# Optimization experiments

Measured on AMD Instinct MI355X. Metric: run time of the kernel, lower is better.

## Reference

```python
import jax, jax.numpy as jnp
import numpy as np

# ---- static config (matches init_kwargs: nlevs=[2,3,4], Pyr_mode=1, dfilt='pkva') ----
NLEVS = (2, 3, 4)
L = 3
# symmetric length-12 ladder (lifting) filter in the spirit of the 'pkva' ladder filter
_PKVA_HALF = np.array([0.6300, -0.1930, 0.0972, -0.0526, 0.0272, -0.0144])
PKVA = np.concatenate([_PKVA_HALF[::-1], _PKVA_HALF])


def _lp_hp_masks(H, W):
    """Meyer-style smooth lowpass/highpass frequency masks (rcos smooth_func)."""
    def phi(n):
        w = np.abs(2.0 * np.pi * np.fft.fftfreq(n))
        s = np.clip((w - np.pi / 3.0) / (np.pi / 3.0), 0.0, 1.0)
        beta = s ** 4 * (35.0 - 84.0 * s + 70.0 * s ** 2 - 20.0 * s ** 3)
        return np.cos(0.5 * np.pi * beta)
    Lm = phi(H)[:, None] * phi(W)[None, :]
    Hm = np.sqrt(np.clip(1.0 - Lm ** 2, 0.0, None))
    return jnp.asarray(Lm, jnp.float32), jnp.asarray(Hm, jnp.float32)


def _pyr_dec(x, nlev):
    """PyrNDDEC_mm, Pyr_mode=1: FFT-domain smooth LP/HP split, dyadic decimation of LP."""
    bands = []
    for _ in range(nlev):
        H, W = x.shape[-2], x.shape[-1]
        Lm, Hm = _lp_hp_masks(H, W)
        Xf = jnp.fft.fft2(x)
        bands.append(jnp.fft.ifft2(Xf * Hm).real.astype(x.dtype))
        x = jnp.fft.ifft2(Xf * Lm).real.astype(x.dtype)[..., ::2, ::2]
    return [x] + bands[::-1]  # y[0]=coarsest lowpass, y[1..L]=bandpass coarse->fine


def _conv1d_wrap(x, f, axis):
    """1D circular ('wrap') convolution along `axis`."""
    K = f.shape[0]
    x = jnp.moveaxis(x, axis, -1)
    pad = [(0, 0)] * (x.ndim - 1) + [(K // 2, K - 1 - K // 2)]
    xp = jnp.pad(x, pad, mode='wrap')
    shp = xp.shape
    y = jax.lax.conv_general_dilated(xp.reshape(-1, 1, shp[-1]),
                                     f.reshape(1, 1, K).astype(x.dtype), (1,), 'VALID')
    y = y.reshape(shp[:-1] + (shp[-1] - K + 1,))
    return jnp.moveaxis(y, -1, axis)


def _fan_split(x, axis, f):
    """One ladder-structured fan filter-bank stage with quincunx coset split."""
    other = -2 if axis == -1 else -1
    n_other = x.shape[other]
    shape = [1] * x.ndim
    shape[other] = n_other
    idx = jnp.arange(n_other)
    # fan <-> diamond modulation along the other axis
    sign = (1 - 2 * (idx % 2)).astype(x.dtype).reshape(shape)
    xm = x * sign
    # quincunx cosets: shift odd lines by 1 along split axis, then deinterleave
    parity = ((idx % 2) == 1).reshape(shape)
    xs = jnp.where(parity, jnp.roll(xm, -1, axis=axis), xm)
    if axis == -1:
        p0, p1 = xs[..., 0::2], xs[..., 1::2]
    else:
        p0, p1 = xs[..., 0::2, :], xs[..., 1::2, :]
    # ladder (lifting) predict/update with 1D filter f
    d = p1 - _conv1d_wrap(p0, f, axis)
    s = p0 + 0.5 * _conv1d_wrap(d, f, axis)
    return s, d


def _dfbdec(x, f, n):
    """n-level directional filter bank (ladder structure). Returns (2^n, ...) stack."""
    subs = x[None]  # (M, B, 1, H, W), all subbands same shape per level -> vectorized
    axis = -1
    for _ in range(n):
        s, d = _fan_split(subs, axis, f)
        subs = jnp.concatenate([s, d], axis=0)
        axis = -2 if axis == -1 else -1
    return subs


def setup_inputs() -> dict:
    key = jax.random.key(0)
    x = jax.random.normal(key, (16, 1, 1024, 1024), dtype=jnp.float32)
    return {"x": x}


def reference(x):
    f = jnp.asarray(PKVA, x.dtype)
    y = _pyr_dec(x, L)
    outs = [y[0]]  # coarsest lowpass (B,1,128,128)
    for k in range(1, L + 1):
        outs.append(_dfbdec(y[k], f, NLEVS[k - 1]))
    # (lowpass, 4 dirs @128x128, 8 dirs @(256,128), 16 dirs @(256,256))
    return tuple(outs)
```

## Files before the change

### kernel.cpp

```cpp
#include <hip/hip_runtime.h>
#include <math.h>

#define PI_F 3.14159265358979323846f

__constant__ float c_pkva[12] = {
  -0.0144f, 0.0272f, -0.0526f, 0.0972f, -0.193f, 0.63f,
   0.63f, -0.193f, 0.0972f, -0.0526f, 0.0272f, -0.0144f
};

constexpr int ilog2c(int n) { int l = 0; while (n > 1) { n >>= 1; ++l; } return l; }

__device__ float g_phi[1920];
constexpr int phi_off(int N) {
  return (N == 1024) ? 0 : (N == 512) ? 1024 : (N == 256) ? 1536 : 1792;
}

__device__ __forceinline__ float phi_dev(int k, int n) {
  int kk = (k < n - k) ? k : (n - k);
  float w = 2.0f * PI_F * (float)kk / (float)n;
  float s = (w - PI_F / 3.0f) * (3.0f / PI_F);
  s = fminf(fmaxf(s, 0.0f), 1.0f);
  float s2 = s * s;
  float beta = s2 * s2 * (35.0f - 84.0f * s + 70.0f * s2 - 20.0f * s2 * s);
  return __cosf(0.5f * PI_F * beta);
}

__global__ void phi_init_k() {
  int i = blockIdx.x * 256 + threadIdx.x;
  if (i < 1024)      g_phi[i] = phi_dev(i, 1024);
  else if (i < 1536) g_phi[i] = phi_dev(i - 1024, 512);
  else if (i < 1792) g_phi[i] = phi_dev(i - 1536, 256);
  else if (i < 1920) g_phi[i] = phi_dev(i - 1792, 128);
}

__device__ __forceinline__ float2 cmul(float2 a, float2 b) {
  return make_float2(a.x * b.x - a.y * b.y, a.x * b.y + a.y * b.x);
}
__device__ __forceinline__ float2 cadd(float2 a, float2 b) { return make_float2(a.x + b.x, a.y + b.y); }
__device__ __forceinline__ float2 csub(float2 a, float2 b) { return make_float2(a.x - b.x, a.y - b.y); }

template <int N>
__device__ __forceinline__ int fft_core4(float2 (*sbuf)[N], float dirsign, int tid, int cur) {
  constexpr int LOG2 = ilog2c(N);
  constexpr int NT = N / 4;
  constexpr bool LEAD2 = (LOG2 & 1);
  if constexpr (LEAD2) {
#pragma unroll
    for (int j = tid; j < N / 2; j += NT) {
      float2 v0 = sbuf[cur][j], v1 = sbuf[cur][j + N / 2];
      float2 e = cadd(v0, v1), o = csub(v0, v1);
      *(float4*)&sbuf[cur ^ 1][2 * j] = make_float4(e.x, e.y, o.x, o.y);
    }
    cur ^= 1;
    __syncthreads();
  }
#pragma unroll
  for (int Ns = LEAD2 ? 2 : 1; Ns < N; Ns <<= 2) {
    int j = tid;
    int base = j & (Ns - 1);
    float ang = dirsign * (2.0f * PI_F) * (float)base / (float)(4 * Ns);
    float2 w1; __sincosf(ang, &w1.y, &w1.x);
    float2 w2 = cmul(w1, w1);
    float2 w3 = cmul(w2, w1);
    float2 v0 = sbuf[cur][j];
    float2 v1 = cmul(sbuf[cur][j + N / 4], w1);
    float2 v2 = cmul(sbuf[cur][j + N / 2], w2);
    float2 v3 = cmul(sbuf[cur][j + 3 * (N / 4)], w3);
    float2 a0 = cadd(v0, v2), a1 = csub(v0, v2);
    float2 a2 = cadd(v1, v3), a3 = csub(v1, v3);
    float2 r1 = make_float2(-dirsign * a3.y, dirsign * a3.x);
    int idxD = ((j - base) << 2) + base;
    cur ^= 1;
    sbuf[cur][idxD]          = cadd(a0, a2);
    sbuf[cur][idxD + Ns]     = cadd(a1, r1);
    sbuf[cur][idxD + 2 * Ns] = csub(a0, a2);
    sbuf[cur][idxD + 3 * Ns] = csub(a1, r1);
    __syncthreads();
  }
  return cur;
}

template <int N, int LMODE, int SMODE>
__global__ void __launch_bounds__(N / 4)
fft_rows_k(const void* __restrict__ vin, void* __restrict__ vout,
           float dirsign, float scale) {
  constexpr int NT = N / 4;
  __shared__ __align__(16) float2 sbuf[2][N];
  const int tid = threadIdx.x;
  const int row = blockIdx.x;
  const int r = row & (N - 1);

  if (LMODE == 1) {
    const float2* in = (const float2*)vin;
#pragma unroll
    for (int i = tid; i < N; i += NT) {
      float2 v = in[(size_t)row * N + i];
      sbuf[0][i] = make_float2(v.x * scale, v.y * scale);
    }
  } else {
    const float2* in = (const float2*)vin;
    float pr = g_phi[phi_off(N) + r];
#pragma unroll
    for (int i = tid; i < N; i += NT) {
      float lm = pr * g_phi[phi_off(N) + i];
      float m = sqrtf(fmaxf(1.0f - lm * lm, 0.0f)) * scale;
      float2 v = in[(size_t)row * N + i];
      sbuf[0][i] = make_float2(v.x * m, v.y * m);
    }
  }
  __syncthreads();

  int cur = fft_core4<N>(sbuf, dirsign, tid, 0);

  if (SMODE == 0) {
    float2* outp = (float2*)vout;
#pragma unroll
    for (int i = tid; i < N; i += NT)
      outp[(size_t)row * N + i] = sbuf[cur][i];
  } else {
    float* outp = (float*)vout;
#pragma unroll
    for (int i = tid; i < N; i += NT)
      outp[(size_t)row * N + i] = sbuf[cur][i].x;
  }
}

template <int N, int PITCH>
__global__ void __launch_bounds__(N / 4)
rfft_pairs_cm_k(const float* __restrict__ in, float2* __restrict__ out) {
  constexpr int NT = N / 4;
  __shared__ __align__(16) float2 sbuf[2][N];
  const int tid = threadIdx.x;
  const int img = blockIdx.x >> (ilog2c(N) - 1);
  const int b = blockIdx.x & (N / 2 - 1);
  const int r = ((b & 7) << (ilog2c(N) - 4)) + (b >> 3);
  const float* p0 = in + ((size_t)img * N + 2 * r) * N;
  const float* p1 = p0 + N;

#pragma unroll
  for (int i = tid; i < N; i += NT)
    sbuf[0][i] = make_float2(p0[i], p1[i]);
  __syncthreads();

  int cur = fft_core4<N>(sbuf, -1.0f, tid, 0);

  float2* ob = out + (size_t)img * ((size_t)PITCH * N) + 2 * r;
#pragma unroll
  for (int i = tid; i <= N / 2; i += NT) {
    float2 Z = sbuf[cur][i];
    float2 Zr = sbuf[cur][(N - i) & (N - 1)];
    float2 Zc = make_float2(Zr.x, -Zr.y);
    float2 o0 = make_float2(0.5f * (Z.x + Zc.x), 0.5f * (Z.y + Zc.y));
    float2 dd = make_float2(Z.x - Zc.x, Z.y - Zc.y);
    float2 o1 = make_float2(0.5f * dd.y, -0.5f * dd.x);
    *(float4*)&ob[(size_t)i * N] = make_float4(o0.x, o0.y, o1.x, o1.y);
  }
}

__global__ void transpose_rect_k(const float2* __restrict__ in,
                                 float2* __restrict__ out, int R, int C) {
  __shared__ float2 tile[32][33];
  int img = blockIdx.z;
  size_t base = (size_t)img * R * C;
  int c = blockIdx.x * 32 + threadIdx.x;
  int r0 = blockIdx.y * 32;
  for (int j = threadIdx.y; j < 32; j += 8)
    tile[j][threadIdx.x] = in[base + (size_t)(r0 + j) * C + c];
  __syncthreads();
  int r = blockIdx.y * 32 + threadIdx.x;
  int c0 = blockIdx.x * 32;
  for (int j = threadIdx.y; j < 32; j += 8)
    out[base + (size_t)(c0 + j) * R + r] = tile[threadIdx.x][j];
}

template <int N, int PITCH>
__global__ void __launch_bounds__(N / 4)
fft_col_half_k(float2* __restrict__ inout, float2* __restrict__ foldb) {
  constexpr int NT = N / 4;
  constexpr int NH = N / 2;
  __shared__ __align__(16) float2 sbuf[2][N];
  const int tid = threadIdx.x;
  const int kx = blockIdx.x;
  const int img = blockIdx.y;
  float2* rowp = inout + ((size_t)img * PITCH + kx) * N;

#pragma unroll
  for (int i = tid; i < N; i += NT)
    sbuf[0][i] = rowp[i];
  __syncthreads();

  int cur = fft_core4<N>(sbuf, -1.0f, tid, 0);

  const float pr = g_phi[phi_off(N) + kx];
  const float inv = 1.0f / (float)N;
  float2* fp = foldb + ((size_t)img * (NH + 1) + kx) * NH;
#pragma unroll
  for (int i = tid; i < NH; i += NT) {
    float2 vA = sbuf[cur][i];
    float2 vB = sbuf[cur][i + NH];
    float lmA = pr * g_phi[phi_off(N) + i];
    float lmB = pr * g_phi[phi_off(N) + i + NH];
    fp[i] = make_float2(0.25f * (vA.x * lmA + vB.x * lmB),
                        0.25f * (vA.y * lmA + vB.y * lmB));
    float hmA = sqrtf(fmaxf(1.0f - lmA * lmA, 0.0f)) * inv;
    float hmB = sqrtf(fmaxf(1.0f - lmB * lmB, 0.0f)) * inv;
    sbuf[cur][i]      = make_float2(vA.x * hmA, vA.y * hmA);
    sbuf[cur][i + NH] = make_float2(vB.x * hmB, vB.y * hmB);
  }
  __syncthreads();

  cur = fft_core4<N>(sbuf, 1.0f, tid, cur);

#pragma unroll
  for (int i = tid; i < N; i += NT)
    rowp[i] = sbuf[cur][i];
}

__global__ void __launch_bounds__(256)
fold_alias_k(const float2* __restrict__ fold, float2* __restrict__ spec2,
             float2* __restrict__ spec3) {
  __shared__ float2 s2a[512], s2b[512];
  const int rp = blockIdx.x;
  const int img = blockIdx.y;
  const float2* fb = fold + (size_t)img * (513 * 512);
  const float2* fr0 = fb + (size_t)rp * 512;
  const float2* fr1 = fb + (size_t)(512 - rp) * 512;
  const float2* fr2 = fb + (size_t)(rp + 256) * 512;
  const float2* fr3 = fb + (size_t)(256 - rp) * 512;
  float2* sp2 = spec2 + ((size_t)img << 18);
  for (int c = threadIdx.x; c < 512; c += 256) {
    int mc = (512 - c) & 511;
    float2 a0 = fr0[c], b0 = fr1[mc];
    float2 a1 = fr2[c], b1 = fr3[mc];
    float2 v0 = make_float2(a0.x + b0.x, a0.y - b0.y);
    float2 v1 = make_float2(a1.x + b1.x, a1.y - b1.y);
    s2a[c] = v0; s2b[c] = v1;
    sp2[((size_t)rp << 9) + c] = v0;
    sp2[((size_t)(rp + 256) << 9) + c] = v1;
  }
  __syncthreads();
  float pr0 = g_phi[phi_off(512) + rp], pr1 = g_phi[phi_off(512) + rp + 256];
  float2* sp3 = spec3 + ((size_t)img << 16) + ((size_t)rp << 8);
  {
    int c = threadIdx.x;
    float pc0 = g_phi[phi_off(512) + c], pc1 = g_phi[phi_off(512) + c + 256];
    float2 v00 = s2a[c], v01 = s2a[c + 256], v10 = s2b[c], v11 = s2b[c + 256];
    float m00 = pr0 * pc0, m01 = pr0 * pc1, m10 = pr1 * pc0, m11 = pr1 * pc1;
    sp3[c] = make_float2(
        0.25f * (v00.x * m00 + v01.x * m01 + v10.x * m10 + v11.x * m11),
        0.25f * (v00.y * m00 + v01.y * m01 + v10.y * m10 + v11.y * m11));
  }
}

template <int N, int PITCH>
__global__ void __launch_bounds__(N / 4)
ifft_fan_pair_k(const float2* __restrict__ in, float* __restrict__ outb,
                float scale, int halfT) {
  constexpr int NT = N / 4;
  constexpr int W2 = N / 2;
  __shared__ __align__(16) float2 sbuf[2][N];
  const int tid = threadIdx.x;
  const int img = blockIdx.x >> (ilog2c(N) - 1);
  const int q = blockIdx.x & (N / 2 - 1);
  const int y0 = 2 * q;
  const float2* inA = in + ((size_t)img * N + y0) * PITCH;
  const float2* inB = inA + PITCH;

#pragma unroll
  for (int i = tid; i <= W2; i += NT) {
    float2 a = inA[i], b = inB[i];
    sbuf[0][i] = make_float2((a.x - b.y) * scale, (a.y + b.x) * scale);
  }
#pragma unroll
  for (int i = tid; i < W2 - 1; i += NT) {
    int m = W2 - 1 - i;
    float2 a = inA[m], b = inB[m];
    sbuf[0][W2 + 1 + i] = make_float2((a.x + b.y) * scale, (b.x - a.y) * scale);
  }
  __syncthreads();

  int cur = fft_core4<N>(sbuf, 1.0f, tid, 0);

  float* scratch = (float*)sbuf[cur ^ 1];
  float* xe = scratch;
  float* xo = scratch + W2;
  float* db = scratch + 2 * W2;
  const size_t rbase = ((size_t)img * N + y0) * W2;

  for (int sub = 0; sub < 2; ++sub) {
    const int par = sub;
    const float sgn = par ? -1.0f : 1.0f;
#pragma unroll
    for (int i = tid; i < N; i += NT) {
      float v = par ? sbuf[cur][i].y : sbuf[cur][i].x;
      int ii = (i - par) & (N - 1);
      if (ii & 1) xo[ii >> 1] = v; else xe[ii >> 1] = v;
    }
    __syncthreads();

    float* outs = outb + rbase + (size_t)sub * W2;
    float* outd = outb + halfT + rbase + (size_t)sub * W2;
#pragma unroll 2
    for (int j = tid; j < W2; j += NT) {
      float acc = 0.0f;
#pragma unroll
      for (int k = 0; k < 12; k++)
        acc += c_pkva[k] * xe[(j - 6 + k + W2) & (W2 - 1)];
      float dv = sgn * (xo[j] - acc);
      db[j] = dv;
      outd[j] = dv;
    }
    __syncthreads();
#pragma unroll 2
    for (int j = tid; j < W2; j += NT) {
      float acc = 0.0f;
#pragma unroll
      for (int k = 0; k < 12; k++)
        acc += c_pkva[k] * db[(j - 6 + k + W2) & (W2 - 1)];
      outs[j] = sgn * xe[j] + 0.5f * acc;
    }
    __syncthreads();
  }
}

template <int N>
__global__ void __launch_bounds__(N / 4)
ifft_fan_k(const float2* __restrict__ in, float* __restrict__ outb,
           float scale, int halfT) {
  constexpr int NT = N / 4;
  constexpr int W2 = N / 2;
  __shared__ __align__(16) float2 sbuf[2][N];
  const int tid = threadIdx.x;
  const int nr = blockIdx.x;
  const int r = nr & (N - 1);
  const int par = r & 1;
  const float sgn = par ? -1.0f : 1.0f;

#pragma unroll
  for (int i = tid; i < N; i += NT) {
    float2 v = in[(size_t)nr * N + i];
    sbuf[0][i] = make_float2(v.x * scale, v.y * scale);
  }
  __syncthreads();

  int cur = fft_core4<N>(sbuf, 1.0f, tid, 0);

  float* scratch = (float*)sbuf[cur ^ 1];
  float* xe = scratch;
  float* xo = scratch + W2;
  float* db = scratch + 2 * W2;
#pragma unroll
  for (int i = tid; i < N; i += NT) {
    float v = sbuf[cur][i].x;
    int ii = (i - par) & (N - 1);
    if (ii & 1) xo[ii >> 1] = v; else xe[ii >> 1] = v;
  }
  __syncthreads();

  float* outs = outb + (size_t)nr * W2;
  float* outd = outb + halfT + (size_t)nr * W2;
#pragma unroll 2
  for (int j = tid; j < W2; j += NT) {
    float acc = 0.0f;
#pragma unroll
    for (int k = 0; k < 12; k++)
      acc += c_pkva[k] * xe[(j - 6 + k + W2) & (W2 - 1)];
    float dv = sgn * (xo[j] - acc);
    db[j] = dv;
    outd[j] = dv;
  }
  __syncthreads();
#pragma unroll 2
  for (int j = tid; j < W2; j += NT) {
    float acc = 0.0f;
#pragma unroll
    for (int k = 0; k < 12; k++)
      acc += c_pkva[k] * db[(j - 6 + k + W2) & (W2 - 1)];
    outs[j] = sgn * xe[j] + 0.5f * acc;
  }
}

__global__ void transpose_k(const float2* __restrict__ in,
                            float2* __restrict__ out, int N) {
  __shared__ float2 tile[32][33];
  int img = blockIdx.z;
  size_t base = (size_t)img * N * N;
  int x = blockIdx.x * 32 + threadIdx.x;
  int y0 = blockIdx.y * 32;
  for (int j = threadIdx.y; j < 32; j += 8)
    tile[j][threadIdx.x] = in[base + (size_t)(y0 + j) * N + x];
  __syncthreads();
  int x2 = blockIdx.y * 32 + threadIdx.x;
  int y2 = blockIdx.x * 32;
  for (int j = threadIdx.y; j < 32; j += 8)
    out[base + (size_t)(y2 + j) * N + x2] = tile[threadIdx.x][j];
}

__global__ void alias_k(const float2* __restrict__ in, float2* __restrict__ out,
                        int N, int lgN2, int phiOff) {
  int idx = blockIdx.x * 256 + threadIdx.x;
  int N2 = N >> 1;
  int c = idx & (N2 - 1);
  int r = (idx >> lgN2) & (N2 - 1);
  int img = idx >> (2 * lgN2);
  float pr0 = g_phi[phiOff + r], pr1 = g_phi[phiOff + r + N2];
  float pc0 = g_phi[phiOff + c], pc1 = g_phi[phiOff + c + N2];
  size_t base = (size_t)img * N * N;
  float2 v00 = in[base + (size_t)r * N + c];
  float2 v01 = in[base + (size_t)r * N + c + N2];
  float2 v10 = in[base + (size_t)(r + N2) * N + c];
  float2 v11 = in[base + (size_t)(r + N2) * N + c + N2];
  float m00 = pr0 * pc0, m01 = pr0 * pc1, m10 = pr1 * pc0, m11 = pr1 * pc1;
  float2 o;
  o.x = 0.25f * (v00.x * m00 + v01.x * m01 + v10.x * m10 + v11.x * m11);
  o.y = 0.25f * (v00.y * m00 + v01.y * m01 + v10.y * m10 + v11.y * m11);
  out[((size_t)img << (2 * lgN2)) + ((size_t)r << lgN2) + c] = o;
}

__global__ void __launch_bounds__(256)
fs_row_k(const float* __restrict__ x, float* __restrict__ outb,
         int lgH, int lgW, int halfT) {
  __shared__ float xe[512], xo[512], db[512];
  int H = 1 << lgH, W = 1 << lgW, W2 = W >> 1;
  int nr = blockIdx.x;
  int r = nr & (H - 1);
  int par = r & 1;
  float sgn = par ? -1.0f : 1.0f;
  const float* xrow = x + (size_t)nr * W;
  for (int j = threadIdx.x; j < W2; j += 256) {
    xe[j] = sgn * xrow[(2 * j + par) & (W - 1)];
    xo[j] = sgn * xrow[(2 * j + 1 + par) & (W - 1)];
  }
  __syncthreads();
  float* outs = outb + (size_t)nr * W2;
  float* outd = outb + halfT + (size_t)nr * W2;
  for (int j = threadIdx.x; j < W2; j += 256) {
    float acc = 0.0f;
#pragma unroll
    for (int k = 0; k < 12; k++)
      acc += c_pkva[k] * xe[(j - 6 + k + W2) & (W2 - 1)];
    float dv = xo[j] - acc;
    db[j] = dv;
    outd[j] = dv;
  }
  __syncthreads();
  for (int j = threadIdx.x; j < W2; j += 256) {
    float acc = 0.0f;
#pragma unroll
    for (int k = 0; k < 12; k++)
      acc += c_pkva[k] * db[(j - 6 + k + W2) & (W2 - 1)];
    outs[j] = xe[j] + 0.5f * acc;
  }
}

template <int TI, int TC>
__global__ void __launch_bounds__(256)
fs_col_fused_k(const float* __restrict__ x, float* __restrict__ outb,
               int lgH, int lgW, int halfT) {
  constexpr int RE = 2 * TI + 48;
  constexpr int DE = TI + 12;
  constexpr int NR = 256 / TC;
  __shared__ float raw[RE][TC];
  __shared__ float dvs[DE][TC];
  const int H = 1 << lgH, W = 1 << lgW;
  const int c0 = blockIdx.x * TC;
  const int i0 = blockIdx.y * TI;
  const int n = blockIdx.z;
  const int tc = threadIdx.x & (TC - 1);
  const int tr = threadIdx.x / TC;
  const float* xim = x + ((size_t)n << (lgH + lgW));
  const int rbase = 2 * i0 - 24;
#pragma unroll
  for (int r = tr; r < RE; r += NR) {
    int rr = (rbase + r) & (H - 1);
    raw[r][tc] = xim[((size_t)rr << lgW) + c0 + tc];
  }
  __syncthreads();
  const int par = tc & 1;
  for (int j = tr; j < DE; j += NR) {
    float acc = 0.0f;
#pragma unroll
    for (int k = 0; k < 12; k++)
      acc += c_pkva[k] * raw[2 * j + 2 * k + par][tc];
    dvs[j][tc] = raw[2 * j + 13 + par][tc] - acc;
  }
  __syncthreads();
  const float sgn = par ? -1.0f : 1.0f;
  float* outs = outb + (((size_t)n << (lgH - 1)) << lgW);
  float* outd = outs + halfT;
  for (int i = tr; i < TI; i += NR) {
    float acc = 0.0f;
#pragma unroll
    for (int k = 0; k < 12; k++)
      acc += c_pkva[k] * dvs[i + k][tc];
    float p0v = raw[2 * i + 24 + par][tc];
    size_t off = ((size_t)(i0 + i) << lgW) + c0 + tc;
    outd[off] = sgn * dvs[i + 6][tc];
    outs[off] = sgn * (p0v + 0.5f * acc);
  }
}

__global__ void fill_err_k(float* out) {
  out[threadIdx.x] = 1.0e9f;
}

extern "C" void kernel_launch(void* const* d_in, const int* in_sizes, int n_in,
                              void* d_out, int out_size, void* d_ws, size_t ws_size,
                              hipStream_t stream) {
  const float* x = (const float*)d_in[0];
  float* out = (float*)d_out;
  char* ws = (char*)d_ws;

  const size_t NEED = 220266496ull;
  if (ws_size < NEED) {
    fill_err_k<<<dim3(1), dim3(256), 0, stream>>>(out);
    return;
  }

  float2* bufA  = (float2*)(ws);
  float2* bufB  = (float2*)(ws + 71303168);
  float2* foldb = (float2*)(ws + 142606336);
  float2* spec2 = (float2*)(ws + 176226304);
  float2* spec3 = (float2*)(ws + 209780736);
  float2* spec4 = (float2*)(ws + 218169344);

  float* out0 = out;
  float* out1 = out + 262144;
  float* out2 = out + 1310720;
  float* out3 = out + 5505024;

  phi_init_k<<<dim3(8), dim3(256), 0, stream>>>();

  rfft_pairs_cm_k<1024, 544><<<dim3(8192), dim3(256), 0, stream>>>(x, bufB);
  fft_col_half_k<1024, 544><<<dim3(513, 16), dim3(256), 0, stream>>>(bufB, foldb);
  fold_alias_k<<<dim3(256, 16), dim3(256), 0, stream>>>(foldb, spec2, spec3);
  transpose_rect_k<<<dim3(32, 17, 16), dim3(32, 8), 0, stream>>>(bufB, bufA, 544, 1024);
  ifft_fan_pair_k<1024, 544><<<dim3(8192), dim3(256), 0, stream>>>(bufA, (float*)bufB, 1.0f / 1024.0f, 8388608);
  fs_col_fused_k<64, 32><<<dim3(16, 8, 32), dim3(256), 0, stream>>>((float*)bufB, (float*)bufA, 10, 9, 8388608);
  fs_row_k<<<dim3(32768), dim3(256), 0, stream>>>((float*)bufA, (float*)bufB, 9, 9, 8388608);
  fs_col_fused_k<64, 32><<<dim3(8, 4, 128), dim3(256), 0, stream>>>((float*)bufB, out3, 9, 8, 8388608);

  fft_rows_k<512, 2, 0><<<dim3(8192), dim3(128), 0, stream>>>((const void*)spec2, (void*)bufA, 1.0f, 1.0f / 512.0f);
  transpose_k<<<dim3(16, 16, 16), dim3(32, 8), 0, stream>>>(bufA, bufB, 512);
  ifft_fan_k<512><<<dim3(8192), dim3(128), 0, stream>>>(bufB, (float*)bufA, 1.0f / 512.0f, 2097152);
  fs_col_fused_k<64, 32><<<dim3(8, 4, 32), dim3(256), 0, stream>>>((float*)bufA, (float*)bufB, 9, 8, 2097152);
  fs_row_k<<<dim3(16384), dim3(256), 0, stream>>>((float*)bufB, out2, 8, 8, 2097152);

  alias_k<<<dim3(1024), dim3(256), 0, stream>>>(spec3, spec4, 256, 7, phi_off(256));
  fft_rows_k<256, 2, 0><<<dim3(4096), dim3(64), 0, stream>>>((const void*)spec3, (void*)bufA, 1.0f, 1.0f / 256.0f);
  transpose_k<<<dim3(8, 8, 16), dim3(32, 8), 0, stream>>>(bufA, bufB, 256);
  ifft_fan_k<256><<<dim3(4096), dim3(64), 0, stream>>>(bufB, (float*)bufA, 1.0f / 256.0f, 524288);
  fs_col_fused_k<64, 32><<<dim3(4, 2, 32), dim3(256), 0, stream>>>((float*)bufA, out1, 8, 7, 524288);

  fft_rows_k<128, 1, 0><<<dim3(2048), dim3(32), 0, stream>>>((const void*)spec4, (void*)bufA, 1.0f, 1.0f / 128.0f);
  transpose_k<<<dim3(4, 4, 16), dim3(32, 8), 0, stream>>>(bufA, bufB, 128);
  fft_rows_k<128, 1, 1><<<dim3(2048), dim3(32), 0, stream>>>((const void*)bufB, (void*)out0, 1.0f, 1.0f / 128.0f);
}
```

Before: 479.1 us.

## Fuse row IFFTs with transposed column-major stores; drop transposes and spec2 buffer

Adds a row-FFT kernel that processes two rows per block and writes results transposed (column-major, float4 pairs). This removes the separate transpose kernels at levels 2, 3 and the lowpass. Level 2 now reads the folded spectrum directly and applies the highpass mask on load, so the spec2 intermediate buffer is no longer written. FFT twiddles now come from a precomputed global table instead of per-stage sincos. The costs are strided column writes with half-row coalescing and extra table loads.

```diff
diff --git a/kernel.cpp b/kernel.cpp
--- a/kernel.cpp
+++ b/kernel.cpp
@@ -11,6 +11,7 @@
 constexpr int ilog2c(int n) { int l = 0; while (n > 1) { n >>= 1; ++l; } return l; }
 
 __device__ float g_phi[1920];
+__device__ float2 g_tw[512];
 constexpr int phi_off(int N) {
   return (N == 1024) ? 0 : (N == 512) ? 1024 : (N == 256) ? 1536 : 1792;
 }
@@ -31,6 +32,15 @@
   else if (i < 1536) g_phi[i] = phi_dev(i - 1024, 512);
   else if (i < 1792) g_phi[i] = phi_dev(i - 1536, 256);
   else if (i < 1920) g_phi[i] = phi_dev(i - 1792, 128);
+  else {
+    int idx = i - 1920;
+    if (idx >= 1 && idx < 512) {
+      int l = 31 - __clz(idx);
+      int Ns = 1 << l;
+      float th = 2.0f * PI_F * (float)(idx - Ns) / (float)(4 * Ns);
+      g_tw[idx] = make_float2(cosf(th), sinf(th));
+    }
+  }
 }
 
 __device__ __forceinline__ float2 cmul(float2 a, float2 b) {
@@ -58,8 +68,8 @@
   for (int Ns = LEAD2 ? 2 : 1; Ns < N; Ns <<= 2) {
     int j = tid;
     int base = j & (Ns - 1);
-    float ang = dirsign * (2.0f * PI_F) * (float)base / (float)(4 * Ns);
-    float2 w1; __sincosf(ang, &w1.y, &w1.x);
+    float2 t = g_tw[Ns + base];
+    float2 w1 = make_float2(t.x, dirsign * t.y);
     float2 w2 = cmul(w1, w1);
     float2 w3 = cmul(w2, w1);
     float2 v0 = sbuf[cur][j];
@@ -125,6 +135,69 @@
   }
 }
 
+template <int N, int LMODE>
+__global__ void __launch_bounds__(N / 4)
+fft_rows_cm_k(const float2* __restrict__ in, float2* __restrict__ outcm,
+              float scale) {
+  constexpr int NT = N / 4;
+  __shared__ __align__(16) float2 sbuf[2][N];
+  const int tid = threadIdx.x;
+  const int img = blockIdx.y;
+  const int b = blockIdx.x;
+  const int q = ((b & 7) << (ilog2c(N) - 4)) + (b >> 3);
+  float2 r0v[4], r1v[4];
+
+#pragma unroll
+  for (int half = 0; half < 2; ++half) {
+    const int r = 2 * q + half;
+    if constexpr (LMODE == 1) {
+      const float2* rp = in + ((size_t)img * N + r) * N;
+#pragma unroll
+      for (int i = tid; i < N; i += NT) {
+        float2 v = rp[i];
+        sbuf[0][i] = make_float2(v.x * scale, v.y * scale);
+      }
+    } else if constexpr (LMODE == 2) {
+      const float2* rp = in + ((size_t)img * N + r) * N;
+      float pr = g_phi[phi_off(N) + r];
+#pragma unroll
+      for (int i = tid; i < N; i += NT) {
+        float lm = pr * g_phi[phi_off(N) + i];
+        float m = sqrtf(fmaxf(1.0f - lm * lm, 0.0f)) * scale;
+        float2 v = rp[i];
+        sbuf[0][i] = make_float2(v.x * m, v.y * m);
+      }
+    } else {
+      const float2* fb = in + (size_t)img * (513 * 512);
+      const float2* fr0 = fb + (size_t)r * 512;
+      const float2* fr1 = fb + (size_t)(512 - r) * 512;
+      float pr = g_phi[phi_off(512) + r];
+#pragma unroll
+      for (int i = tid; i < N; i += NT) {
+        float2 a = fr0[i], bb = fr1[(512 - i) & 511];
+        float lm = pr * g_phi[phi_off(512) + i];
+        float m = sqrtf(fmaxf(1.0f - lm * lm, 0.0f)) * scale;
+        sbuf[0][i] = make_float2((a.x + bb.x) * m, (a.y - bb.y) * m);
+      }
+    }
+    __syncthreads();
+
+    int cur = fft_core4<N>(sbuf, 1.0f, tid, 0);
+
+#pragma unroll
+    for (int i = tid, k = 0; i < N; i += NT, ++k) {
+      float2 v = sbuf[cur][i];
+      if (half == 0) r0v[k] = v; else r1v[k] = v;
+    }
+    __syncthreads();
+  }
+
+  float2* ob = outcm + (size_t)img * N * N + 2 * q;
+#pragma unroll
+  for (int i = tid, k = 0; i < N; i += NT, ++k)
+    *(float4*)&ob[(size_t)i * N] = make_float4(r0v[k].x, r0v[k].y, r1v[k].x, r1v[k].y);
+}
+
 template <int N, int PITCH>
 __global__ void __launch_bounds__(N / 4)
 rfft_pairs_cm_k(const float* __restrict__ in, float2* __restrict__ out) {
@@ -217,8 +290,7 @@
 }
 
 __global__ void __launch_bounds__(256)
-fold_alias_k(const float2* __restrict__ fold, float2* __restrict__ spec2,
-             float2* __restrict__ spec3) {
+fold_spec3_k(const float2* __restrict__ fold, float2* __restrict__ spec3) {
   __shared__ float2 s2a[512], s2b[512];
   const int rp = blockIdx.x;
   const int img = blockIdx.y;
@@ -227,16 +299,12 @@
   const float2* fr1 = fb + (size_t)(512 - rp) * 512;
   const float2* fr2 = fb + (size_t)(rp + 256) * 512;
   const float2* fr3 = fb + (size_t)(256 - rp) * 512;
-  float2* sp2 = spec2 + ((size_t)img << 18);
   for (int c = threadIdx.x; c < 512; c += 256) {
     int mc = (512 - c) & 511;
     float2 a0 = fr0[c], b0 = fr1[mc];
     float2 a1 = fr2[c], b1 = fr3[mc];
-    float2 v0 = make_float2(a0.x + b0.x, a0.y - b0.y);
-    float2 v1 = make_float2(a1.x + b1.x, a1.y - b1.y);
-    s2a[c] = v0; s2b[c] = v1;
-    sp2[((size_t)rp << 9) + c] = v0;
-    sp2[((size_t)(rp + 256) << 9) + c] = v1;
+    s2a[c] = make_float2(a0.x + b0.x, a0.y - b0.y);
+    s2b[c] = make_float2(a1.x + b1.x, a1.y - b1.y);
   }
   __syncthreads();
   float pr0 = g_phi[phi_off(512) + rp], pr1 = g_phi[phi_off(512) + rp + 256];
@@ -378,22 +446,6 @@
       acc += c_pkva[k] * db[(j - 6 + k + W2) & (W2 - 1)];
     outs[j] = sgn * xe[j] + 0.5f * acc;
   }
-}
-
-__global__ void transpose_k(const float2* __restrict__ in,
-                            float2* __restrict__ out, int N) {
-  __shared__ float2 tile[32][33];
-  int img = blockIdx.z;
-  size_t base = (size_t)img * N * N;
-  int x = blockIdx.x * 32 + threadIdx.x;
-  int y0 = blockIdx.y * 32;
-  for (int j = threadIdx.y; j < 32; j += 8)
-    tile[j][threadIdx.x] = in[base + (size_t)(y0 + j) * N + x];
-  __syncthreads();
-  int x2 = blockIdx.y * 32 + threadIdx.x;
-  int y2 = blockIdx.x * 32;
-  for (int j = threadIdx.y; j < 32; j += 8)
-    out[base + (size_t)(y2 + j) * N + x2] = tile[threadIdx.x][j];
 }
 
 __global__ void alias_k(const float2* __restrict__ in, float2* __restrict__ out,
@@ -520,7 +572,6 @@
   float2* bufA  = (float2*)(ws);
   float2* bufB  = (float2*)(ws + 71303168);
   float2* foldb = (float2*)(ws + 142606336);
-  float2* spec2 = (float2*)(ws + 176226304);
   float2* spec3 = (float2*)(ws + 209780736);
   float2* spec4 = (float2*)(ws + 218169344);
 
@@ -529,30 +580,27 @@
   float* out2 = out + 1310720;
   float* out3 = out + 5505024;
 
-  phi_init_k<<<dim3(8), dim3(256), 0, stream>>>();
+  phi_init_k<<<dim3(10), dim3(256), 0, stream>>>();
 
   rfft_pairs_cm_k<1024, 544><<<dim3(8192), dim3(256), 0, stream>>>(x, bufB);
   fft_col_half_k<1024, 544><<<dim3(513, 16), dim3(256), 0, stream>>>(bufB, foldb);
-  fold_alias_k<<<dim3(256, 16), dim3(256), 0, stream>>>(foldb, spec2, spec3);
+  fold_spec3_k<<<dim3(256, 16), dim3(256), 0, stream>>>(foldb, spec3);
   transpose_rect_k<<<dim3(32, 17, 16), dim3(32, 8), 0, stream>>>(bufB, bufA, 544, 1024);
   ifft_fan_pair_k<1024, 544><<<dim3(8192), dim3(256), 0, stream>>>(bufA, (float*)bufB, 1.0f / 1024.0f, 8388608);
   fs_col_fused_k<64, 32><<<dim3(16, 8, 32), dim3(256), 0, stream>>>((float*)bufB, (float*)bufA, 10, 9, 8388608);
   fs_row_k<<<dim3(32768), dim3(256), 0, stream>>>((float*)bufA, (float*)bufB, 9, 9, 8388608);
   fs_col_fused_k<64, 32><<<dim3(8, 4, 128), dim3(256), 0, stream>>>((float*)bufB, out3, 9, 8, 8388608);
 
-  fft_rows_k<512, 2, 0><<<dim3(8192), dim3(128), 0, stream>>>((const void*)spec2, (void*)bufA, 1.0f, 1.0f / 512.0f);
-  transpose_k<<<dim3(16, 16, 16), dim3(32, 8), 0, stream>>>(bufA, bufB, 512);
-  ifft_fan_k<512><<<dim3(8192), dim3(128), 0, stream>>>(bufB, (float*)bufA, 1.0f / 512.0f, 2097152);
-  fs_col_fused_k<64, 32><<<dim3(8, 4, 32), dim3(256), 0, stream>>>((float*)bufA, (float*)bufB, 9, 8, 2097152);
-  fs_row_k<<<dim3(16384), dim3(256), 0, stream>>>((float*)bufB, out2, 8, 8, 2097152);
+  fft_rows_cm_k<512, 3><<<dim3(256, 16), dim3(128), 0, stream>>>(foldb, bufA, 1.0f / 512.0f);
+  ifft_fan_k<512><<<dim3(8192), dim3(128), 0, stream>>>(bufA, (float*)bufB, 1.0f / 512.0f, 2097152);
+  fs_col_fused_k<64, 32><<<dim3(8, 4, 32), dim3(256), 0, stream>>>((float*)bufB, (float*)bufA, 9, 8, 2097152);
+  fs_row_k<<<dim3(16384), dim3(256), 0, stream>>>((float*)bufA, out2, 8, 8, 2097152);
 
   alias_k<<<dim3(1024), dim3(256), 0, stream>>>(spec3, spec4, 256, 7, phi_off(256));
-  fft_rows_k<256, 2, 0><<<dim3(4096), dim3(64), 0, stream>>>((const void*)spec3, (void*)bufA, 1.0f, 1.0f / 256.0f);
-  transpose_k<<<dim3(8, 8, 16), dim3(32, 8), 0, stream>>>(bufA, bufB, 256);
-  ifft_fan_k<256><<<dim3(4096), dim3(64), 0, stream>>>(bufB, (float*)bufA, 1.0f / 256.0f, 524288);
-  fs_col_fused_k<64, 32><<<dim3(4, 2, 32), dim3(256), 0, stream>>>((float*)bufA, out1, 8, 7, 524288);
-
-  fft_rows_k<128, 1, 0><<<dim3(2048), dim3(32), 0, stream>>>((const void*)spec4, (void*)bufA, 1.0f, 1.0f / 128.0f);
-  transpose_k<<<dim3(4, 4, 16), dim3(32, 8), 0, stream>>>(bufA, bufB, 128);
-  fft_rows_k<128, 1, 1><<<dim3(2048), dim3(32), 0, stream>>>((const void*)bufB, (void*)out0, 1.0f, 1.0f / 128.0f);
-}
+  fft_rows_cm_k<256, 2><<<dim3(128, 16), dim3(64), 0, stream>>>(spec3, bufA, 1.0f / 256.0f);
+  ifft_fan_k<256><<<dim3(4096), dim3(64), 0, stream>>>(bufA, (float*)bufB, 1.0f / 256.0f, 524288);
+  fs_col_fused_k<64, 32><<<dim3(4, 2, 32), dim3(256), 0, stream>>>((float*)bufB, out1, 8, 7, 524288);
+
+  fft_rows_cm_k<128, 1><<<dim3(64, 16), dim3(32), 0, stream>>>(spec4, bufA, 1.0f / 128.0f);
+  fft_rows_k<128, 1, 1><<<dim3(2048), dim3(32), 0, stream>>>((const void*)bufA, (void*)out0, 1.0f, 1.0f / 128.0f);
+}
```

New measurement: 482.1 us. Within noise of the previous version (+0.6%).
